# Kernel tuning notes

Measured on AMD Instinct MI355X. Metric: run time of the kernel, lower is better.

Reference implementation:

```python
import jax, jax.numpy as jnp
import numpy as np

N = 50000   # nodes
E = 100000  # directed edges
G = 2048    # graphs in batch
D = 32      # hidden dim
F_NODE = 11
F_EDGE = 4


def setup_inputs() -> dict:
    key = jax.random.key(0)
    ks = jax.random.split(key, 12)
    s = 0.1
    return {
        "x": jax.random.normal(ks[0], (N, F_NODE), dtype=jnp.float32),
        "edge_attr": jax.random.uniform(ks[1], (E, F_EDGE), dtype=jnp.float32),
        "lin0_w": jax.random.normal(ks[2], (D, F_NODE), dtype=jnp.float32) * s,
        "lin0_b": jnp.zeros((D,), jnp.float32),
        "nn_w": jax.random.normal(ks[3], (D * D, F_EDGE), dtype=jnp.float32) * s,
        "nn_b": jnp.zeros((D * D,), jnp.float32),
        "root_w": jax.random.normal(ks[4], (D, D), dtype=jnp.float32) * s,
        "conv_b": jnp.zeros((D,), jnp.float32),
        "gru_wi": jax.random.normal(ks[5], (3 * D, D), dtype=jnp.float32) * s,
        "gru_wh": jax.random.normal(ks[6], (3 * D, D), dtype=jnp.float32) * s,
        "gru_bi": jnp.zeros((3 * D,), jnp.float32),
        "gru_bh": jnp.zeros((3 * D,), jnp.float32),
        "lin1_w": jax.random.normal(ks[7], (2, D), dtype=jnp.float32) * s,
        "lin1_b": jnp.zeros((2,), jnp.float32),
        "edge_index": jax.random.randint(ks[8], (2, E), 0, N, dtype=jnp.int32),
        "batch": jnp.sort(jax.random.randint(ks[9], (N,), 0, G, dtype=jnp.int32)),
    }


def _gru_step(m, h, wi, wh, bi, bh):
    # single-step torch.nn.GRU cell math
    gi = m @ wi.T + bi            # [N, 3D]
    gh = h @ wh.T + bh            # [N, 3D]
    ir, iz, inn = jnp.split(gi, 3, axis=-1)
    hr, hz, hn = jnp.split(gh, 3, axis=-1)
    r = jax.nn.sigmoid(ir + hr)
    z = jax.nn.sigmoid(iz + hz)
    n = jnp.tanh(inn + r * hn)
    return (1.0 - z) * n + z * h


def reference(x, edge_attr, lin0_w, lin0_b, nn_w, nn_b, root_w, conv_b,
              gru_wi, gru_wh, gru_bi, gru_bh, lin1_w, lin1_b,
              edge_index, batch):
    src, dst = edge_index[0], edge_index[1]
    out = jax.nn.relu(x @ lin0_w.T + lin0_b)   # [N, D]
    h = out
    # per-edge 32x32 weight from edge MLP (edge_attr fixed -> hoisted out of loop)
    W_e = (edge_attr @ nn_w.T + nn_b).reshape(E, D, D)
    for _ in range(3):
        msg = jnp.einsum('ei,eio->eo', out[src], W_e)                  # [E, D]
        aggr = jax.ops.segment_sum(msg, dst, num_segments=N)           # add-aggregate
        m = jax.nn.relu(aggr + out @ root_w + conv_b)                  # NNConv root + bias
        h = _gru_step(m, h, gru_wi, gru_wh, gru_bi, gru_bh)
        out = h
    cnt = jax.ops.segment_sum(jnp.ones((N,), x.dtype), batch, num_segments=G)
    pooled = jax.ops.segment_sum(out, batch, num_segments=G) / jnp.maximum(cnt, 1.0)[:, None]
    logits = pooled @ lin1_w.T + lin1_b                                # [G, 2]
    return jax.nn.log_softmax(logits, axis=1)
```

## Files before the change

### kernel.cpp

```cpp
#include <hip/hip_runtime.h>
#include <hip/hip_bf16.h>

#define NN 50000
#define EE 100000
#define GG 2048
#define NB_SCAN 196

__device__ __forceinline__ float b2f(unsigned short u) {
    union { unsigned int i; float f; } x; x.i = (unsigned int)u << 16; return x.f;
}
__device__ __forceinline__ unsigned short f2b(float f) {
    union { float f; unsigned int i; } x; x.f = f;
    unsigned int b = x.i + (0x7FFFu + ((x.i >> 16) & 1u));
    return (unsigned short)(b >> 16);
}

__global__ void k_init(const float* __restrict__ x, const float* __restrict__ w,
                       const float* __restrict__ b, float* __restrict__ feat) {
    int idx = blockIdx.x * blockDim.x + threadIdx.x;
    if (idx >= NN * 32) return;
    int n = idx >> 5, o = idx & 31;
    const float* xr = x + n * 11;
    const float* wr = w + o * 11;
    float acc = b[o];
#pragma unroll
    for (int i = 0; i < 11; ++i) acc += xr[i] * wr[i];
    feat[idx] = fmaxf(acc, 0.f);
}

__global__ void k_prep(const float* __restrict__ nnw, const float* __restrict__ nnb,
                       const float* __restrict__ wi, const float* __restrict__ wh,
                       float* __restrict__ Wre, float* __restrict__ WyT,
                       float* __restrict__ wiT, float* __restrict__ whT) {
    int idx = blockIdx.x * blockDim.x + threadIdx.x;
    if (idx < 5120) {
        int c = idx >> 5, i = idx & 31;
        float v;
        if (c < 128) v = nnw[((i << 5) + (c & 31)) * 4 + (c >> 5)];
        else         v = nnb[(i << 5) + (c - 128)];
        Wre[idx] = v;
    } else if (idx < 10240) {
        int j = idx - 5120;
        int i = j / 160, c = j - i * 160;
        float v;
        if (c < 128) v = nnw[((i << 5) + (c & 31)) * 4 + (c >> 5)];
        else         v = nnb[(i << 5) + (c - 128)];
        WyT[j] = v;
    } else if (idx < 13312) {
        int j = idx - 10240;
        int k = j / 96, c = j - k * 96;
        wiT[j] = wi[c * 32 + k];
    } else if (idx < 16384) {
        int j = idx - 13312;
        int k = j / 96, c = j - k * 96;
        whT[j] = wh[c * 32 + k];
    }
}

__global__ void k_hist(const int* __restrict__ ei, int* __restrict__ cnt) {
    int e = blockIdx.x * blockDim.x + threadIdx.x;
    if (e >= EE) return;
    atomicAdd(&cnt[ei[EE + e]], 1);
}

__global__ __launch_bounds__(256) void k_scan1(const int* __restrict__ cnt,
                                               int* __restrict__ tmp,
                                               int* __restrict__ bsum) {
    __shared__ int sd[256];
    int t = threadIdx.x;
    int i = blockIdx.x * 256 + t;
    int v = (i < NN) ? cnt[i] : 0;
    sd[t] = v;
    __syncthreads();
#pragma unroll
    for (int off = 1; off < 256; off <<= 1) {
        int x = (t >= off) ? sd[t - off] : 0;
        __syncthreads();
        sd[t] += x;
        __syncthreads();
    }
    if (i < NN) tmp[i] = sd[t];
    if (t == 255) bsum[blockIdx.x] = sd[255];
}

__global__ __launch_bounds__(256) void k_scan2(int* __restrict__ bsum) {
    __shared__ int sd[256];
    int t = threadIdx.x;
    int v = (t < NB_SCAN) ? bsum[t] : 0;
    sd[t] = v;
    __syncthreads();
#pragma unroll
    for (int off = 1; off < 256; off <<= 1) {
        int x = (t >= off) ? sd[t - off] : 0;
        __syncthreads();
        sd[t] += x;
        __syncthreads();
    }
    if (t < NB_SCAN) bsum[t] = sd[t];
}

__global__ void k_scan3(const int* __restrict__ cnt, const int* __restrict__ tmp,
                        const int* __restrict__ bsum, int* __restrict__ row_ptr,
                        int* __restrict__ cursor) {
    int i = blockIdx.x * blockDim.x + threadIdx.x;
    if (i >= NN) return;
    int base = (blockIdx.x > 0) ? bsum[blockIdx.x - 1] : 0;
    int excl = base + tmp[i] - cnt[i];
    row_ptr[i] = excl;
    cursor[i] = excl;
    if (i == 0) row_ptr[NN] = EE;
}

__global__ void k_scatter(const int* __restrict__ ei, const float* __restrict__ ea,
                          int* __restrict__ cursor, int* __restrict__ esrc,
                          float4* __restrict__ eea) {
    int e = blockIdx.x * blockDim.x + threadIdx.x;
    if (e >= EE) return;
    int d = ei[EE + e];
    int slot = atomicAdd(&cursor[d], 1);
    esrc[slot] = ei[e];
    eea[slot] = make_float4(ea[e * 4 + 0], ea[e * 4 + 1], ea[e * 4 + 2], ea[e * 4 + 3]);
}

__global__ __launch_bounds__(256) void k_y(const float* __restrict__ feat,
                                           const float* __restrict__ Wre,
                                           unsigned short* __restrict__ yb) {
    int lane = threadIdx.x & 63;
    int wv = __builtin_amdgcn_readfirstlane(threadIdx.x >> 6);
    int n = blockIdx.x * 64 + lane;
    if (n >= NN) return;
    int c0 = blockIdx.y * 40 + wv * 10;
    float fr[32];
    const float4* f4 = (const float4*)(feat + (long)n * 32);
#pragma unroll
    for (int q = 0; q < 8; ++q) {
        float4 v = f4[q];
        fr[4 * q + 0] = v.x; fr[4 * q + 1] = v.y;
        fr[4 * q + 2] = v.z; fr[4 * q + 3] = v.w;
    }
    float acc[10];
#pragma unroll
    for (int cc = 0; cc < 10; ++cc) {
        const float* w = Wre + (c0 + cc) * 32;
        float a = 0.f;
#pragma unroll
        for (int i = 0; i < 32; ++i) a += fr[i] * w[i];
        acc[cc] = a;
    }
    unsigned short* yr = yb + (long)n * 160 + c0;
#pragma unroll
    for (int q = 0; q < 5; ++q) {
        unsigned int wlo = f2b(acc[2 * q]);
        unsigned int whi = f2b(acc[2 * q + 1]);
        ((unsigned int*)yr)[q] = wlo | (whi << 16);
    }
}

__global__ __launch_bounds__(256) void k_msg(
    const unsigned short* __restrict__ yb, const int* __restrict__ esrc,
    const float4* __restrict__ eea, float* __restrict__ msg) {
    int idx = blockIdx.x * 256 + threadIdx.x;
    if (idx >= EE * 32) return;
    int slot = idx >> 5, o = idx & 31;
    int s = esrc[slot];
    float4 a = eea[slot];
    const unsigned short* yr = yb + (long)s * 160;
    float y0 = b2f(yr[o]);
    float y1 = b2f(yr[32 + o]);
    float y2 = b2f(yr[64 + o]);
    float y3 = b2f(yr[96 + o]);
    float y4 = b2f(yr[128 + o]);
    msg[idx] = y4 + a.x * y0 + a.y * y1 + a.z * y2 + a.w * y3;
}

__global__ __launch_bounds__(256) void k_conv_update(
    const float* __restrict__ msg, const int* __restrict__ row_ptr,
    const float* __restrict__ rootw, const float* __restrict__ convb,
    const float* __restrict__ wiT, const float* __restrict__ whT,
    const float* __restrict__ bi, const float* __restrict__ bh,
    const float* __restrict__ WyT, float* __restrict__ feat,
    unsigned short* __restrict__ yb, int write_y) {
    __shared__ float fs[32][32];
    __shared__ float ms[32][32];
    int t = threadIdx.x;
    int g = t >> 5, o = t & 31;
    int nb = blockIdx.x * 32 + g * 4;
    float f[4], m[4];
#pragma unroll
    for (int j = 0; j < 4; ++j) {
        int n = nb + j;
        bool v = (n < NN);
        f[j] = v ? feat[(long)n * 32 + o] : 0.f;
        fs[g * 4 + j][o] = f[j];
        m[j] = convb[o];
        if (v) {
            int e0 = row_ptr[n], e1 = row_ptr[n + 1];
            for (int e = e0; e < e1; ++e)
                m[j] += msg[((long)e << 5) + o];
        }
    }
    __syncthreads();
#pragma unroll 4
    for (int i = 0; i < 32; ++i) {
        float rw = rootw[i * 32 + o];
#pragma unroll
        for (int j = 0; j < 4; ++j) m[j] += fs[g * 4 + j][i] * rw;
    }
#pragma unroll
    for (int j = 0; j < 4; ++j) {
        m[j] = fmaxf(m[j], 0.f);
        ms[g * 4 + j][o] = m[j];
    }
    __syncthreads();
    float bir = bi[o], biz = bi[32 + o], bin_ = bi[64 + o];
    float bhr = bh[o], bhz = bh[32 + o], bhn = bh[64 + o];
    float gir[4], giz[4], gin_[4], ghr[4], ghz[4], ghn[4];
#pragma unroll
    for (int j = 0; j < 4; ++j) {
        gir[j] = bir; giz[j] = biz; gin_[j] = bin_;
        ghr[j] = bhr; ghz[j] = bhz; ghn[j] = bhn;
    }
#pragma unroll 2
    for (int k = 0; k < 32; ++k) {
        const float* wik = wiT + k * 96 + o;
        const float* whk = whT + k * 96 + o;
        float wir = wik[0], wiz = wik[32], win = wik[64];
        float whr = whk[0], whz = whk[32], whn = whk[64];
#pragma unroll
        for (int j = 0; j < 4; ++j) {
            float mk = ms[g * 4 + j][k], hk = fs[g * 4 + j][k];
            gir[j] += mk * wir;
            giz[j] += mk * wiz;
            gin_[j] += mk * win;
            ghr[j] += hk * whr;
            ghz[j] += hk * whz;
            ghn[j] += hk * whn;
        }
    }
    float fn[4];
#pragma unroll
    for (int j = 0; j < 4; ++j) {
        int n = nb + j;
        float r = 1.f / (1.f + __expf(-(gir[j] + ghr[j])));
        float z = 1.f / (1.f + __expf(-(giz[j] + ghz[j])));
        float nt = tanhf(gin_[j] + r * ghn[j]);
        fn[j] = (1.f - z) * nt + z * f[j];
        if (n < NN) feat[(long)n * 32 + o] = fn[j];
    }
    if (!write_y) return;
#pragma unroll
    for (int j = 0; j < 4; ++j) fs[g * 4 + j][o] = fn[j];
    float ya[4][5];
#pragma unroll
    for (int j = 0; j < 4; ++j)
#pragma unroll
        for (int q = 0; q < 5; ++q) ya[j][q] = 0.f;
#pragma unroll 4
    for (int i = 0; i < 32; ++i) {
        const float* wy = WyT + i * 160 + o;
        float w0 = wy[0], w1 = wy[32], w2 = wy[64], w3 = wy[96], w4 = wy[128];
#pragma unroll
        for (int j = 0; j < 4; ++j) {
            float fv = fs[g * 4 + j][i];
            ya[j][0] += fv * w0;
            ya[j][1] += fv * w1;
            ya[j][2] += fv * w2;
            ya[j][3] += fv * w3;
            ya[j][4] += fv * w4;
        }
    }
#pragma unroll
    for (int j = 0; j < 4; ++j) {
        int n = nb + j;
        if (n < NN) {
            unsigned short* yr = yb + (long)n * 160 + o;
#pragma unroll
            for (int q = 0; q < 5; ++q) yr[q * 32] = f2b(ya[j][q]);
        }
    }
}

__global__ __launch_bounds__(64) void k_pool_final(
    const float* __restrict__ feat, const int* __restrict__ batch,
    const float* __restrict__ w, const float* __restrict__ b,
    float* __restrict__ out) {
    int g = blockIdx.x;
    int t = threadIdx.x;
    int o = t & 31, h = t >> 5;
    int lo = 0, hi = NN;
    while (lo < hi) { int mid = (lo + hi) >> 1; if (batch[mid] < g) lo = mid + 1; else hi = mid; }
    int start = lo;
    hi = NN;
    while (lo < hi) { int mid = (lo + hi) >> 1; if (batch[mid] <= g) lo = mid + 1; else hi = mid; }
    int end = lo;
    float acc = 0.f;
    for (int n = start + h; n < end; n += 2) acc += feat[(long)n * 32 + o];
    acc += __shfl_xor(acc, 32, 64);
    float p = acc / fmaxf((float)(end - start), 1.f);
    float l0 = p * w[o], l1 = p * w[32 + o];
#pragma unroll
    for (int s = 16; s >= 1; s >>= 1) {
        l0 += __shfl_xor(l0, s, 64);
        l1 += __shfl_xor(l1, s, 64);
    }
    if (t == 0) {
        l0 += b[0]; l1 += b[1];
        float mx = fmaxf(l0, l1);
        float lse = mx + logf(__expf(l0 - mx) + __expf(l1 - mx));
        out[g * 2 + 0] = l0 - lse;
        out[g * 2 + 1] = l1 - lse;
    }
}

extern "C" void kernel_launch(void* const* d_in, const int* in_sizes, int n_in,
                              void* d_out, int out_size, void* d_ws, size_t ws_size,
                              hipStream_t stream) {
    const float* x        = (const float*)d_in[0];
    const float* edge_attr= (const float*)d_in[1];
    const float* lin0_w   = (const float*)d_in[2];
    const float* lin0_b   = (const float*)d_in[3];
    const float* nn_w     = (const float*)d_in[4];
    const float* nn_b     = (const float*)d_in[5];
    const float* root_w   = (const float*)d_in[6];
    const float* conv_b   = (const float*)d_in[7];
    const float* gru_wi   = (const float*)d_in[8];
    const float* gru_wh   = (const float*)d_in[9];
    const float* gru_bi   = (const float*)d_in[10];
    const float* gru_bh   = (const float*)d_in[11];
    const float* lin1_w   = (const float*)d_in[12];
    const float* lin1_b   = (const float*)d_in[13];
    const int*   edge_idx = (const int*)d_in[14];
    const int*   batch    = (const int*)d_in[15];
    float* out = (float*)d_out;

    float* ws     = (float*)d_ws;
    float* feat   = ws;
    float* Wre    = feat + (long)NN * 32;
    float* WyT    = Wre + 5120;
    float* wiT    = WyT + 5120;
    float* whT    = wiT + 3072;
    int*   row_cnt= (int*)(whT + 3072);
    int*   tmp    = row_cnt + NN;
    int*   bsum   = tmp + NN;
    int*   row_ptr= bsum + 256;
    int*   cursor = row_ptr + NN + 1;
    int*   esrc   = cursor + NN;
    size_t off = ((size_t)((char*)(esrc + EE) - (char*)d_ws) + 15) & ~(size_t)15;
    float4* eea  = (float4*)((char*)d_ws + off);
    unsigned short* yb = (unsigned short*)(eea + EE);
    float* msg   = (float*)(yb + (long)NN * 160);

    hipMemsetAsync(row_cnt, 0, NN * sizeof(int), stream);

    k_prep<<<64, 256, 0, stream>>>(nn_w, nn_b, gru_wi, gru_wh, Wre, WyT, wiT, whT);
    k_init<<<(NN * 32 + 255) / 256, 256, 0, stream>>>(x, lin0_w, lin0_b, feat);

    k_hist<<<(EE + 255) / 256, 256, 0, stream>>>(edge_idx, row_cnt);
    k_scan1<<<NB_SCAN, 256, 0, stream>>>(row_cnt, tmp, bsum);
    k_scan2<<<1, 256, 0, stream>>>(bsum);
    k_scan3<<<NB_SCAN, 256, 0, stream>>>(row_cnt, tmp, bsum, row_ptr, cursor);
    k_scatter<<<(EE + 255) / 256, 256, 0, stream>>>(edge_idx, edge_attr, cursor, esrc, eea);

    dim3 gy((NN + 63) / 64, 4);
    k_y<<<gy, 256, 0, stream>>>(feat, Wre, yb);
    for (int it = 0; it < 3; ++it) {
        k_msg<<<(EE * 32 + 255) / 256, 256, 0, stream>>>(yb, esrc, eea, msg);
        k_conv_update<<<(NN + 31) / 32, 256, 0, stream>>>(msg, row_ptr,
                                                          root_w, conv_b, wiT, whT,
                                                          gru_bi, gru_bh, WyT,
                                                          feat, yb, it < 2 ? 1 : 0);
    }

    k_pool_final<<<GG, 64, 0, stream>>>(feat, batch, lin1_w, lin1_b, out);
}
```

Before: 304.9 us.

## Fuse per-edge message computation into node update via source-side CSR push

Builds a second CSR keyed by source node (a combined histogram and scan over both directions) that records each edge's dst-sorted slot and attributes. Each node-update kernel then writes its outgoing edge messages straight into the ping-pong message buffer, so the separate k_msg launch and the bf16 y round-trip disappear in iterations two and three. The cost is extra scatter work at setup and scattered 32-float writes per edge from the update kernel. The per-node loop over out-edges adds divergence and load imbalance in a kernel that is already heavy on registers.

```diff
diff --git a/kernel.cpp b/kernel.cpp
--- a/kernel.cpp
+++ b/kernel.cpp
@@ -4,7 +4,7 @@
 #define NN 50000
 #define EE 100000
 #define GG 2048
-#define NB_SCAN 196
+#define NB2 391
 
 __device__ __forceinline__ float b2f(unsigned short u) {
     union { unsigned int i; float f; } x; x.i = (unsigned int)u << 16; return x.f;
@@ -61,6 +61,7 @@
     int e = blockIdx.x * blockDim.x + threadIdx.x;
     if (e >= EE) return;
     atomicAdd(&cnt[ei[EE + e]], 1);
+    atomicAdd(&cnt[NN + ei[e]], 1);
 }
 
 __global__ __launch_bounds__(256) void k_scan1(const int* __restrict__ cnt,
@@ -69,7 +70,7 @@
     __shared__ int sd[256];
     int t = threadIdx.x;
     int i = blockIdx.x * 256 + t;
-    int v = (i < NN) ? cnt[i] : 0;
+    int v = (i < 2 * NN) ? cnt[i] : 0;
     sd[t] = v;
     __syncthreads();
 #pragma unroll
@@ -79,47 +80,60 @@
         sd[t] += x;
         __syncthreads();
     }
-    if (i < NN) tmp[i] = sd[t];
+    if (i < 2 * NN) tmp[i] = sd[t];
     if (t == 255) bsum[blockIdx.x] = sd[255];
 }
 
-__global__ __launch_bounds__(256) void k_scan2(int* __restrict__ bsum) {
-    __shared__ int sd[256];
+__global__ __launch_bounds__(512) void k_scan2(int* __restrict__ bsum) {
+    __shared__ int sd[512];
     int t = threadIdx.x;
-    int v = (t < NB_SCAN) ? bsum[t] : 0;
+    int v = (t < NB2) ? bsum[t] : 0;
     sd[t] = v;
     __syncthreads();
 #pragma unroll
-    for (int off = 1; off < 256; off <<= 1) {
+    for (int off = 1; off < 512; off <<= 1) {
         int x = (t >= off) ? sd[t - off] : 0;
         __syncthreads();
         sd[t] += x;
         __syncthreads();
     }
-    if (t < NB_SCAN) bsum[t] = sd[t];
+    if (t < NB2) bsum[t] = sd[t];
 }
 
 __global__ void k_scan3(const int* __restrict__ cnt, const int* __restrict__ tmp,
                         const int* __restrict__ bsum, int* __restrict__ row_ptr,
-                        int* __restrict__ cursor) {
+                        int* __restrict__ cursor, int* __restrict__ out_ptr,
+                        int* __restrict__ cursor2) {
     int i = blockIdx.x * blockDim.x + threadIdx.x;
-    if (i >= NN) return;
+    if (i >= 2 * NN) return;
     int base = (blockIdx.x > 0) ? bsum[blockIdx.x - 1] : 0;
     int excl = base + tmp[i] - cnt[i];
-    row_ptr[i] = excl;
-    cursor[i] = excl;
-    if (i == 0) row_ptr[NN] = EE;
+    if (i < NN) {
+        row_ptr[i] = excl;
+        cursor[i] = excl;
+        if (i == 0) row_ptr[NN] = EE;
+    } else {
+        int j = i - NN;
+        out_ptr[j] = excl - EE;
+        cursor2[j] = excl - EE;
+        if (j == 0) out_ptr[NN] = EE;
+    }
 }
 
 __global__ void k_scatter(const int* __restrict__ ei, const float* __restrict__ ea,
-                          int* __restrict__ cursor, int* __restrict__ esrc,
-                          float4* __restrict__ eea) {
+                          int* __restrict__ cursor, int* __restrict__ cursor2,
+                          int* __restrict__ esrc, float4* __restrict__ eea,
+                          int* __restrict__ oslot, float4* __restrict__ oea) {
     int e = blockIdx.x * blockDim.x + threadIdx.x;
     if (e >= EE) return;
-    int d = ei[EE + e];
+    int s = ei[e], d = ei[EE + e];
+    float4 a = make_float4(ea[e * 4 + 0], ea[e * 4 + 1], ea[e * 4 + 2], ea[e * 4 + 3]);
     int slot = atomicAdd(&cursor[d], 1);
-    esrc[slot] = ei[e];
-    eea[slot] = make_float4(ea[e * 4 + 0], ea[e * 4 + 1], ea[e * 4 + 2], ea[e * 4 + 3]);
+    esrc[slot] = s;
+    eea[slot] = a;
+    int pos = atomicAdd(&cursor2[s], 1);
+    oslot[pos] = slot;
+    oea[pos] = a;
 }
 
 __global__ __launch_bounds__(256) void k_y(const float* __restrict__ feat,
@@ -174,12 +188,13 @@
 }
 
 __global__ __launch_bounds__(256) void k_conv_update(
-    const float* __restrict__ msg, const int* __restrict__ row_ptr,
+    const float* __restrict__ msg_in, const int* __restrict__ row_ptr,
     const float* __restrict__ rootw, const float* __restrict__ convb,
     const float* __restrict__ wiT, const float* __restrict__ whT,
     const float* __restrict__ bi, const float* __restrict__ bh,
-    const float* __restrict__ WyT, float* __restrict__ feat,
-    unsigned short* __restrict__ yb, int write_y) {
+    const float* __restrict__ WyT, const int* __restrict__ out_ptr,
+    const int* __restrict__ oslot, const float4* __restrict__ oea,
+    float* __restrict__ feat, float* __restrict__ msg_out, int write_msg) {
     __shared__ float fs[32][32];
     __shared__ float ms[32][32];
     int t = threadIdx.x;
@@ -196,7 +211,7 @@
         if (v) {
             int e0 = row_ptr[n], e1 = row_ptr[n + 1];
             for (int e = e0; e < e1; ++e)
-                m[j] += msg[((long)e << 5) + o];
+                m[j] += msg_in[((long)e << 5) + o];
         }
     }
     __syncthreads();
@@ -247,7 +262,7 @@
         fn[j] = (1.f - z) * nt + z * f[j];
         if (n < NN) feat[(long)n * 32 + o] = fn[j];
     }
-    if (!write_y) return;
+    if (!write_msg) return;
 #pragma unroll
     for (int j = 0; j < 4; ++j) fs[g * 4 + j][o] = fn[j];
     float ya[4][5];
@@ -273,9 +288,14 @@
     for (int j = 0; j < 4; ++j) {
         int n = nb + j;
         if (n < NN) {
-            unsigned short* yr = yb + (long)n * 160 + o;
-#pragma unroll
-            for (int q = 0; q < 5; ++q) yr[q * 32] = f2b(ya[j][q]);
+            int p0 = out_ptr[n], p1 = out_ptr[n + 1];
+            for (int p = p0; p < p1; ++p) {
+                float4 a = oea[p];
+                int slot = oslot[p];
+                msg_out[((long)slot << 5) + o] =
+                    ya[j][4] + a.x * ya[j][0] + a.y * ya[j][1]
+                             + a.z * ya[j][2] + a.w * ya[j][3];
+            }
         }
     }
 }
@@ -339,37 +359,50 @@
     float* WyT    = Wre + 5120;
     float* wiT    = WyT + 5120;
     float* whT    = wiT + 3072;
-    int*   row_cnt= (int*)(whT + 3072);
-    int*   tmp    = row_cnt + NN;
-    int*   bsum   = tmp + NN;
-    int*   row_ptr= bsum + 256;
+    int*   cnt    = (int*)(whT + 3072);
+    int*   tmp    = cnt + 2 * NN;
+    int*   bsum   = tmp + 2 * NN;
+    int*   row_ptr= bsum + 512;
     int*   cursor = row_ptr + NN + 1;
-    int*   esrc   = cursor + NN;
-    size_t off = ((size_t)((char*)(esrc + EE) - (char*)d_ws) + 15) & ~(size_t)15;
+    int*   out_ptr= cursor + NN;
+    int*   cursor2= out_ptr + NN + 1;
+    int*   esrc   = cursor2 + NN;
+    int*   oslot  = esrc + EE;
+    size_t off = ((size_t)((char*)(oslot + EE) - (char*)d_ws) + 15) & ~(size_t)15;
     float4* eea  = (float4*)((char*)d_ws + off);
-    unsigned short* yb = (unsigned short*)(eea + EE);
-    float* msg   = (float*)(yb + (long)NN * 160);
-
-    hipMemsetAsync(row_cnt, 0, NN * sizeof(int), stream);
+    float4* oea  = eea + EE;
+    unsigned short* yb = (unsigned short*)(oea + EE);
+    float* msgA  = (float*)(yb + (long)NN * 160);
+    float* msgB  = msgA + (long)EE * 32;
+
+    hipMemsetAsync(cnt, 0, 2 * NN * sizeof(int), stream);
 
     k_prep<<<64, 256, 0, stream>>>(nn_w, nn_b, gru_wi, gru_wh, Wre, WyT, wiT, whT);
     k_init<<<(NN * 32 + 255) / 256, 256, 0, stream>>>(x, lin0_w, lin0_b, feat);
 
-    k_hist<<<(EE + 255) / 256, 256, 0, stream>>>(edge_idx, row_cnt);
-    k_scan1<<<NB_SCAN, 256, 0, stream>>>(row_cnt, tmp, bsum);
-    k_scan2<<<1, 256, 0, stream>>>(bsum);
-    k_scan3<<<NB_SCAN, 256, 0, stream>>>(row_cnt, tmp, bsum, row_ptr, cursor);
-    k_scatter<<<(EE + 255) / 256, 256, 0, stream>>>(edge_idx, edge_attr, cursor, esrc, eea);
+    k_hist<<<(EE + 255) / 256, 256, 0, stream>>>(edge_idx, cnt);
+    k_scan1<<<NB2, 256, 0, stream>>>(cnt, tmp, bsum);
+    k_scan2<<<1, 512, 0, stream>>>(bsum);
+    k_scan3<<<NB2, 256, 0, stream>>>(cnt, tmp, bsum, row_ptr, cursor, out_ptr, cursor2);
+    k_scatter<<<(EE + 255) / 256, 256, 0, stream>>>(edge_idx, edge_attr, cursor, cursor2,
+                                                    esrc, eea, oslot, oea);
 
     dim3 gy((NN + 63) / 64, 4);
     k_y<<<gy, 256, 0, stream>>>(feat, Wre, yb);
-    for (int it = 0; it < 3; ++it) {
-        k_msg<<<(EE * 32 + 255) / 256, 256, 0, stream>>>(yb, esrc, eea, msg);
-        k_conv_update<<<(NN + 31) / 32, 256, 0, stream>>>(msg, row_ptr,
-                                                          root_w, conv_b, wiT, whT,
-                                                          gru_bi, gru_bh, WyT,
-                                                          feat, yb, it < 2 ? 1 : 0);
-    }
+    k_msg<<<(EE * 32 + 255) / 256, 256, 0, stream>>>(yb, esrc, eea, msgA);
+
+    k_conv_update<<<(NN + 31) / 32, 256, 0, stream>>>(msgA, row_ptr, root_w, conv_b,
+                                                      wiT, whT, gru_bi, gru_bh, WyT,
+                                                      out_ptr, oslot, oea,
+                                                      feat, msgB, 1);
+    k_conv_update<<<(NN + 31) / 32, 256, 0, stream>>>(msgB, row_ptr, root_w, conv_b,
+                                                      wiT, whT, gru_bi, gru_bh, WyT,
+                                                      out_ptr, oslot, oea,
+                                                      feat, msgA, 1);
+    k_conv_update<<<(NN + 31) / 32, 256, 0, stream>>>(msgA, row_ptr, root_w, conv_b,
+                                                      wiT, whT, gru_bi, gru_bh, WyT,
+                                                      out_ptr, oslot, oea,
+                                                      feat, msgB, 0);
 
     k_pool_final<<<GG, 64, 0, stream>>>(feat, batch, lin1_w, lin1_b, out);
 }
```

New measurement: 293.0 us. -3.9%, faster.
